# Optimization experiments

Measured on AMD Instinct MI355X. Metric: run time of the kernel, lower is better.

The kernel has to match this reference:

```python
import jax, jax.numpy as jnp
import numpy as np

B, S, H = 4, 2048, 1024
HEADS = 16
DFF = 4 * H
EPS = 1e-12


def _layer_norm(x, w, b):
    mu = jnp.mean(x, axis=-1, keepdims=True)
    var = jnp.mean(jnp.square(x - mu), axis=-1, keepdims=True)
    return (x - mu) * jax.lax.rsqrt(var + EPS) * w + b


def setup_inputs() -> dict:
    key = jax.random.key(0)
    ks = jax.random.split(key, 12)
    sc = 0.02
    return {
        "input": jax.random.normal(ks[0], (B, S, H), dtype=jnp.float32),
        "input_mask": jnp.zeros((B, 1, 1, S), dtype=jnp.float32),
        "norm_w": jnp.ones((H,), jnp.float32),
        "norm_b": jnp.zeros((H,), jnp.float32),
        "qkv_w": sc * jax.random.normal(ks[1], (H, 3 * H), jnp.float32),
        "qkv_b": jnp.zeros((3 * H,), jnp.float32),
        "attn_ow": sc * jax.random.normal(ks[2], (H, H), jnp.float32),
        "attn_ob": jnp.zeros((H,), jnp.float32),
        "attn_nw": jnp.ones((H,), jnp.float32),
        "attn_nb": jnp.zeros((H,), jnp.float32),
        "inter_w": sc * jax.random.normal(ks[3], (H, DFF), jnp.float32),
        "inter_b": jnp.zeros((DFF,), jnp.float32),
        "output_w": sc * jax.random.normal(ks[4], (DFF, H), jnp.float32),
        "output_b": jnp.zeros((H,), jnp.float32),
    }


def reference(input, input_mask, norm_w, norm_b, qkv_w, qkv_b, attn_ow, attn_ob,
              attn_nw, attn_nb, inter_w, inter_b, output_w, output_b):
    b, s, h = input.shape
    hd = h // HEADS
    # pre-LN + fused QKV projection (qkv_func)
    x_ln = _layer_norm(input, norm_w, norm_b)
    qkv = x_ln @ qkv_w + qkv_b                      # [b, s, 3h]
    qkv = qkv.reshape(b, s, 3, HEADS, hd)
    q, k, v = qkv[:, :, 0], qkv[:, :, 1], qkv[:, :, 2]   # [b, s, heads, hd]
    # scaled dot-product attention (flash_attn equivalent, non-causal)
    scale = 1.0 / jnp.sqrt(jnp.float32(hd))
    scores = jnp.einsum('bqnd,bknd->bnqk', q, k) * scale  # [b, heads, s, s]
    scores = scores + input_mask                           # additive mask
    probs = jax.nn.softmax(scores, axis=-1)
    ctx = jnp.einsum('bnqk,bknd->bqnd', probs, v).reshape(b, s, h)
    # attention output projection + residual (mlp_func first half)
    attn_out = ctx @ attn_ow + attn_ob + input
    # post-attention LN + FFN (GELU) + residual
    y = _layer_norm(attn_out, attn_nw, attn_nb)
    y = jax.nn.gelu(y @ inter_w + inter_b, approximate=False)
    return y @ output_w + output_b + attn_out
```

## Files before the change

kernel.cpp:

```cpp
#include <hip/hip_runtime.h>
#include <math.h>

typedef __bf16 bf16_t;
typedef bf16_t bf16x8 __attribute__((ext_vector_type(8)));
typedef bf16_t bf16x4 __attribute__((ext_vector_type(4)));
typedef float f32x4 __attribute__((ext_vector_type(4)));
typedef float f32x16 __attribute__((ext_vector_type(16)));

#define BB 4
#define SS 2048
#define HD1 1024
#define NH 16
#define DFF_ 4096

__device__ __forceinline__ void gload_lds16(const bf16_t* g, bf16_t* l) {
  __builtin_amdgcn_global_load_lds(
      (const __attribute__((address_space(1))) void*)g,
      (__attribute__((address_space(3))) void*)l, 16, 0, 0);
}

__device__ __forceinline__ unsigned pack2_bf16(float a, float b) {
  union { bf16_t h[2]; unsigned u; } cv;
  cv.h[0] = (bf16_t)a;
  cv.h[1] = (bf16_t)b;
  return cv.u;
}

__device__ __forceinline__ float block_reduce_sum(float v, float* red) {
  const int lane = threadIdx.x & 63;
  const int wid = threadIdx.x >> 6;
#pragma unroll
  for (int off = 32; off > 0; off >>= 1) v += __shfl_down(v, off, 64);
  if (lane == 0) red[wid] = v;
  __syncthreads();
  float s = red[0] + red[1] + red[2] + red[3];
  __syncthreads();
  return s;
}

__global__ __launch_bounds__(256) void ln_kernel(const float* __restrict__ x,
                                                 const float* __restrict__ w,
                                                 const float* __restrict__ bv,
                                                 bf16_t* __restrict__ out) {
  __shared__ float red[4];
  const size_t row = blockIdx.x;
  const float4 xv = *(const float4*)(x + row * HD1 + threadIdx.x * 4);
  float s = xv.x + xv.y + xv.z + xv.w;
  s = block_reduce_sum(s, red);
  const float mu = s * (1.0f / HD1);
  float4 d;
  d.x = xv.x - mu; d.y = xv.y - mu; d.z = xv.z - mu; d.w = xv.w - mu;
  float sq = d.x * d.x + d.y * d.y + d.z * d.z + d.w * d.w;
  sq = block_reduce_sum(sq, red);
  const float rs = rsqrtf(sq * (1.0f / HD1) + 1e-12f);
  const float4 wv = *(const float4*)(w + threadIdx.x * 4);
  const float4 bb = *(const float4*)(bv + threadIdx.x * 4);
  bf16x4 o;
  o[0] = (bf16_t)(d.x * rs * wv.x + bb.x);
  o[1] = (bf16_t)(d.y * rs * wv.y + bb.y);
  o[2] = (bf16_t)(d.z * rs * wv.z + bb.z);
  o[3] = (bf16_t)(d.w * rs * wv.w + bb.w);
  *(bf16x4*)(out + row * HD1 + threadIdx.x * 4) = o;
}

__global__ __launch_bounds__(256) void wt_kernel(const float* __restrict__ W,
                                                 bf16_t* __restrict__ Wt,
                                                 int K, int N) {
  __shared__ bf16_t T[32][33];
  const int t = threadIdx.x;
  const int n0 = blockIdx.x * 32, k0 = blockIdx.y * 32;
  const int a = t >> 5, c = t & 31;
#pragma unroll
  for (int i = 0; i < 4; ++i) {
    const int kl = a + i * 8;
    T[kl][c] = (bf16_t)W[(size_t)(k0 + kl) * N + n0 + c];
  }
  __syncthreads();
#pragma unroll
  for (int i = 0; i < 4; ++i) {
    const int nl = a + i * 8;
    Wt[(size_t)(n0 + nl) * K + k0 + c] = T[c][nl];
  }
}

__global__ __launch_bounds__(256) void vtrans_kernel(const bf16_t* __restrict__ qkv,
                                                     bf16_t* __restrict__ Vt) {
  const int t = threadIdx.x;
  const int s = blockIdx.x * 256 + t;
  const int head = blockIdx.y, b = blockIdx.z;
  const bf16_t* src = qkv + (size_t)(b * SS + s) * 3072 + 2048 + head * 64;
  bf16_t* dst = Vt + ((size_t)(b * NH + head) * 64) * SS + s;
#pragma unroll
  for (int j = 0; j < 8; ++j) {
    bf16x8 v = *(const bf16x8*)(src + j * 8);
#pragma unroll
    for (int e = 0; e < 8; ++e) dst[(size_t)(j * 8 + e) * SS] = v[e];
  }
}

template <int EPI, bool OBF>
__global__ __launch_bounds__(256) void gemm_bf16(
    const bf16_t* __restrict__ A, const bf16_t* __restrict__ Wt,
    const float* __restrict__ bias, const float* __restrict__ R,
    void* __restrict__ Cout, int M, int N, int K) {
  __shared__ __align__(16) char smem[65536];
  bf16_t* As = (bf16_t*)smem;
  bf16_t* Bs = (bf16_t*)(smem + 32768);
  const int tid = threadIdx.x;
  const int lane = tid & 63;
  const int w = tid >> 6;
  const int wm = (w >> 1) * 64, wn = (w & 1) * 64;
  const int l15 = lane & 15, l4 = lane >> 4;

  const int gx = gridDim.x;
  int id = blockIdx.x + gx * blockIdx.y;
  const int cpx = (gx * gridDim.y) >> 3;
  id = (id & 7) * cpx + (id >> 3);
  const int m0 = (id / gx) * 128;
  const int n0 = (id % gx) * 128;

  const int lrow = tid >> 3;
  const int lcol = (((tid & 7) ^ ((tid >> 3) & 7)) * 8);
  const bf16_t* Ag = A + (size_t)(m0 + lrow) * K + lcol;
  const bf16_t* Bg = Wt + (size_t)(n0 + lrow) * K + lcol;
  const size_t rstride = (size_t)32 * K;

#pragma unroll
  for (int c = 0; c < 4; ++c) {
    gload_lds16(Ag + c * rstride, As + c * 2048 + w * 512);
    gload_lds16(Bg + c * rstride, Bs + c * 2048 + w * 512);
  }

  const int NT = K >> 6;
  f32x4 acc[4][4] = {};

  const int ch0 = (((0 * 4 + l4) ^ (l15 & 7)) * 8);
  const int ch1 = (((1 * 4 + l4) ^ (l15 & 7)) * 8);

  for (int t = 0; t < NT; ++t) {
    const int cur = t & 1;
    __syncthreads();
    if (t + 1 < NT) {
      const bf16_t* Agn = Ag + (size_t)(t + 1) * 64;
      const bf16_t* Bgn = Bg + (size_t)(t + 1) * 64;
      bf16_t* Ad = As + (cur ^ 1) * 8192;
      bf16_t* Bd = Bs + (cur ^ 1) * 8192;
#pragma unroll
      for (int c = 0; c < 4; ++c) {
        gload_lds16(Agn + c * rstride, Ad + c * 2048 + w * 512);
        gload_lds16(Bgn + c * rstride, Bd + c * 2048 + w * 512);
      }
    }
    const bf16_t* Ab = As + cur * 8192;
    const bf16_t* Bb = Bs + cur * 8192;
    bf16x8 af[2][4], bfr[2][4];
#pragma unroll
    for (int i = 0; i < 4; ++i) {
      af[0][i] = *(const bf16x8*)(Ab + (wm + i * 16 + l15) * 64 + ch0);
      af[1][i] = *(const bf16x8*)(Ab + (wm + i * 16 + l15) * 64 + ch1);
    }
#pragma unroll
    for (int j = 0; j < 4; ++j) {
      bfr[0][j] = *(const bf16x8*)(Bb + (wn + j * 16 + l15) * 64 + ch0);
      bfr[1][j] = *(const bf16x8*)(Bb + (wn + j * 16 + l15) * 64 + ch1);
    }
#pragma unroll
    for (int ks = 0; ks < 2; ++ks)
#pragma unroll
      for (int i = 0; i < 4; ++i)
#pragma unroll
        for (int j = 0; j < 4; ++j)
          acc[i][j] = __builtin_amdgcn_mfma_f32_16x16x32_bf16(
              af[ks][i], bfr[ks][j], acc[i][j], 0, 0, 0);
  }

  if (OBF) {
    __syncthreads();
    float* Cs = (float*)smem;
#pragma unroll
    for (int j = 0; j < 4; ++j) {
      const float bj = bias[n0 + wn + j * 16 + l15];
#pragma unroll
      for (int i = 0; i < 4; ++i)
#pragma unroll
        for (int r = 0; r < 4; ++r) {
          float v = acc[i][j][r] + bj;
          if (EPI == 1)
            v = 0.5f * v * (1.0f + erff(v * 0.70710678118654752440f));
          Cs[(wm + i * 16 + l4 * 4 + r) * 128 + wn + j * 16 + l15] = v;
        }
    }
    __syncthreads();
    bf16_t* Cb = (bf16_t*)Cout;
#pragma unroll
    for (int p = 0; p < 16; ++p) {
      const int idx = p * 256 + tid;
      const int row = idx >> 5, c4 = idx & 31;
      const f32x4 v = *(const f32x4*)(Cs + row * 128 + c4 * 4);
      bf16x4 o;
      o[0] = (bf16_t)v[0]; o[1] = (bf16_t)v[1];
      o[2] = (bf16_t)v[2]; o[3] = (bf16_t)v[3];
      *(bf16x4*)(Cb + (size_t)(m0 + row) * N + n0 + c4 * 4) = o;
    }
  } else {
    float* Cf = (float*)Cout;
#pragma unroll
    for (int j = 0; j < 4; ++j) {
      const int gn = n0 + wn + j * 16 + l15;
      const float bj = bias[gn];
#pragma unroll
      for (int i = 0; i < 4; ++i) {
        const int gm = m0 + wm + i * 16 + l4 * 4;
#pragma unroll
        for (int r = 0; r < 4; ++r) {
          float v = acc[i][j][r] + bj;
          if (EPI == 2) v += R[(size_t)(gm + r) * N + gn];
          Cf[(size_t)(gm + r) * N + gn] = v;
        }
      }
    }
  }
}

__global__ __launch_bounds__(256, 3) void attn_kernel(
    const bf16_t* __restrict__ qkv, const bf16_t* __restrict__ Vt,
    const float* __restrict__ mask, bf16_t* __restrict__ ctx) {
  __shared__ __align__(16) bf16_t K_lds[64 * 72];
  __shared__ __align__(16) bf16_t Vt_lds[64 * 72];
  const int tid = threadIdx.x;
  const int lane = tid & 63;
  const int w = tid >> 6;
  const int l31 = lane & 31;
  const int h = lane >> 5;
  const int q0 = blockIdx.x * 128;
  const int head = blockIdx.y;
  const int b = blockIdx.z;
  const int qrow = q0 + w * 32 + l31;

  bf16x8 qf[4];
  {
    const bf16_t* qp = qkv + (size_t)(b * SS + qrow) * 3072 + head * 64 + 8 * h;
#pragma unroll
    for (int ks = 0; ks < 4; ++ks) qf[ks] = *(const bf16x8*)(qp + 16 * ks);
  }

  const int srow = tid >> 2;
  const int scol = (tid & 3) * 16;
  const float* mbase = mask + (size_t)b * SS;

  float m = -3.0e38f, l = 0.0f;
  f32x16 cacc0 = {};
  f32x16 cacc1 = {};

  for (int kv0 = 0; kv0 < SS; kv0 += 64) {
    const bf16_t* kp =
        qkv + (size_t)(b * SS + kv0 + srow) * 3072 + 1024 + head * 64 + scol;
    const bf16_t* vp =
        Vt + ((size_t)(b * NH + head) * 64 + srow) * SS + kv0 + scol;
    const bf16x8 k0 = *(const bf16x8*)kp;
    const bf16x8 k1 = *(const bf16x8*)(kp + 8);
    const bf16x8 v0 = *(const bf16x8*)vp;
    const bf16x8 v1 = *(const bf16x8*)(vp + 8);
    __syncthreads();
    *(bf16x8*)(K_lds + srow * 72 + scol) = k0;
    *(bf16x8*)(K_lds + srow * 72 + scol + 8) = k1;
    *(bf16x8*)(Vt_lds + srow * 72 + scol) = v0;
    *(bf16x8*)(Vt_lds + srow * 72 + scol + 8) = v1;
    __syncthreads();

    f32x16 sacc0 = {};
    f32x16 sacc1 = {};
#pragma unroll
    for (int ks = 0; ks < 4; ++ks) {
      const bf16x8 kf0 = *(const bf16x8*)(K_lds + l31 * 72 + 16 * ks + 8 * h);
      const bf16x8 kf1 =
          *(const bf16x8*)(K_lds + (l31 + 32) * 72 + 16 * ks + 8 * h);
      sacc0 = __builtin_amdgcn_mfma_f32_32x32x16_bf16(kf0, qf[ks], sacc0, 0, 0, 0);
      sacc1 = __builtin_amdgcn_mfma_f32_32x32x16_bf16(kf1, qf[ks], sacc1, 0, 0, 0);
    }

    float ps[32];
    float tmax = -3.0e38f;
#pragma unroll
    for (int r = 0; r < 16; ++r) {
      const int krow = (r & 3) + 8 * (r >> 2) + 4 * h;
      const float s0 = sacc0[r] * 0.125f + mbase[kv0 + krow];
      const float s1 = sacc1[r] * 0.125f + mbase[kv0 + 32 + krow];
      ps[r] = s0;
      ps[16 + r] = s1;
      tmax = fmaxf(tmax, fmaxf(s0, s1));
    }
    tmax = fmaxf(tmax, __shfl_xor(tmax, 32, 64));
    if (__any(tmax > m + 8.0f)) {
      const float mnew = fmaxf(m, tmax);
      const float sc = __expf(m - mnew);
      m = mnew;
      l *= sc;
#pragma unroll
      for (int r = 0; r < 16; ++r) {
        const float scr = __shfl(sc, (r & 3) + 8 * (r >> 2) + 4 * h, 64);
        cacc0[r] *= scr;
        cacc1[r] *= scr;
      }
    }
    float ls = 0.0f;
#pragma unroll
    for (int i = 0; i < 32; ++i) {
      ps[i] = __expf(ps[i] - m);
      ls += ps[i];
    }
    l += ls + __shfl_xor(ls, 32, 64);

    unsigned pw0[8], pw1[8];
#pragma unroll
    for (int k = 0; k < 8; ++k) {
      const int base = (k >> 2) * 16 + (k & 3) * 4;
      pw0[k] = pack2_bf16(ps[base + 0], ps[base + 1]);
      pw1[k] = pack2_bf16(ps[base + 2], ps[base + 3]);
    }
#pragma unroll
    for (int t = 0; t < 4; ++t) {
      const unsigned e0 = h ? pw0[2 * t] : pw0[2 * t + 1];
      const unsigned e1 = h ? pw1[2 * t] : pw1[2 * t + 1];
      const unsigned o0 = (unsigned)__shfl_xor((int)e0, 32, 64);
      const unsigned o1 = (unsigned)__shfl_xor((int)e1, 32, 64);
      const unsigned a0 = h ? pw0[2 * t + 1] : pw0[2 * t];
      const unsigned a1 = h ? pw1[2 * t + 1] : pw1[2 * t];
      union { unsigned u[4]; bf16x8 v; } pu;
      pu.u[0] = h ? o0 : a0;
      pu.u[1] = h ? o1 : a1;
      pu.u[2] = h ? a0 : o0;
      pu.u[3] = h ? a1 : o1;
      const bf16x8 vf0 = *(const bf16x8*)(Vt_lds + l31 * 72 + 16 * t + 8 * h);
      const bf16x8 vf1 =
          *(const bf16x8*)(Vt_lds + (l31 + 32) * 72 + 16 * t + 8 * h);
      cacc0 = __builtin_amdgcn_mfma_f32_32x32x16_bf16(pu.v, vf0, cacc0, 0, 0, 0);
      cacc1 = __builtin_amdgcn_mfma_f32_32x32x16_bf16(pu.v, vf1, cacc1, 0, 0, 0);
    }
  }

  const float linv = 1.0f / l;
#pragma unroll
  for (int r = 0; r < 16; ++r) {
    const int rq = (r & 3) + 8 * (r >> 2) + 4 * h;
    const float li = __shfl(linv, rq, 64);
    const int grow = q0 + w * 32 + rq;
    bf16_t* op = ctx + (size_t)(b * SS + grow) * 1024 + head * 64 + l31;
    op[0] = (bf16_t)(cacc0[r] * li);
    op[32] = (bf16_t)(cacc1[r] * li);
  }
}

extern "C" void kernel_launch(void* const* d_in, const int* in_sizes, int n_in,
                              void* d_out, int out_size, void* d_ws, size_t ws_size,
                              hipStream_t stream) {
  const float* input    = (const float*)d_in[0];
  const float* mask     = (const float*)d_in[1];
  const float* norm_w   = (const float*)d_in[2];
  const float* norm_b   = (const float*)d_in[3];
  const float* qkv_w    = (const float*)d_in[4];
  const float* qkv_b    = (const float*)d_in[5];
  const float* attn_ow  = (const float*)d_in[6];
  const float* attn_ob  = (const float*)d_in[7];
  const float* attn_nw  = (const float*)d_in[8];
  const float* attn_nb  = (const float*)d_in[9];
  const float* inter_w  = (const float*)d_in[10];
  const float* inter_b  = (const float*)d_in[11];
  const float* output_w = (const float*)d_in[12];
  const float* output_b = (const float*)d_in[13];

  char* ws = (char*)d_ws;
  const size_t off_xln = 0;
  const size_t off_qkv = 16777216;
  const size_t off_vt  = 67108864;
  const size_t off_ctx = 83886080;
  const size_t off_ao  = 100663296;
  const size_t off_wq  = 134217728;
  const size_t off_wo  = 140509184;
  const size_t off_wi  = 142606336;
  const size_t off_w2  = 150994944;
  const size_t NEED    = 159383552;
  if (ws_size < NEED) return;

  bf16_t* x_ln  = (bf16_t*)(ws + off_xln);
  bf16_t* qkvb  = (bf16_t*)(ws + off_qkv);
  bf16_t* VtB   = (bf16_t*)(ws + off_vt);
  bf16_t* ctxb  = (bf16_t*)(ws + off_ctx);
  bf16_t* y_ln  = (bf16_t*)(ws + off_ctx);
  float*  a_out = (float*)(ws + off_ao);
  bf16_t* wq_t  = (bf16_t*)(ws + off_wq);
  bf16_t* wo_t  = (bf16_t*)(ws + off_wo);
  bf16_t* wi_t  = (bf16_t*)(ws + off_wi);
  bf16_t* w2_t  = (bf16_t*)(ws + off_w2);
  bf16_t* act   = (bf16_t*)(ws + off_xln);

  const int M = BB * SS;

  wt_kernel<<<dim3(3072 / 32, 1024 / 32), 256, 0, stream>>>(qkv_w, wq_t, 1024, 3072);
  wt_kernel<<<dim3(1024 / 32, 1024 / 32), 256, 0, stream>>>(attn_ow, wo_t, 1024, 1024);
  wt_kernel<<<dim3(4096 / 32, 1024 / 32), 256, 0, stream>>>(inter_w, wi_t, 1024, 4096);
  wt_kernel<<<dim3(1024 / 32, 4096 / 32), 256, 0, stream>>>(output_w, w2_t, 4096, 1024);

  ln_kernel<<<M, 256, 0, stream>>>(input, norm_w, norm_b, x_ln);
  gemm_bf16<0, true><<<dim3(3072 / 128, M / 128), 256, 0, stream>>>(
      x_ln, wq_t, qkv_b, nullptr, qkvb, M, 3072, 1024);
  vtrans_kernel<<<dim3(SS / 256, NH, BB), 256, 0, stream>>>(qkvb, VtB);
  attn_kernel<<<dim3(SS / 128, NH, BB), 256, 0, stream>>>(qkvb, VtB, mask, ctxb);
  gemm_bf16<2, false><<<dim3(1024 / 128, M / 128), 256, 0, stream>>>(
      ctxb, wo_t, attn_ob, input, a_out, M, 1024, 1024);
  ln_kernel<<<M, 256, 0, stream>>>(a_out, attn_nw, attn_nb, y_ln);
  gemm_bf16<1, true><<<dim3(4096 / 128, M / 128), 256, 0, stream>>>(
      y_ln, wi_t, inter_b, nullptr, act, M, 4096, 1024);
  gemm_bf16<2, false><<<dim3(1024 / 128, M / 128), 256, 0, stream>>>(
      act, w2_t, output_b, a_out, (float*)d_out, M, 1024, 4096);
}
```

Baseline: 490.2 us.

## Prefetch K/V tiles into registers, vectorize mask loads, and tile V transpose through LDS

```diff
diff --git a/kernel.cpp b/kernel.cpp
--- a/kernel.cpp
+++ b/kernel.cpp
@@ -20,10 +20,9 @@
 }
 
 __device__ __forceinline__ unsigned pack2_bf16(float a, float b) {
-  union { bf16_t h[2]; unsigned u; } cv;
-  cv.h[0] = (bf16_t)a;
-  cv.h[1] = (bf16_t)b;
-  return cv.u;
+  unsigned r;
+  asm("v_cvt_pk_bf16_f32 %0, %1, %2" : "=v"(r) : "v"(a), "v"(b));
+  return r;
 }
 
 __device__ __forceinline__ float block_reduce_sum(float v, float* red) {
@@ -85,16 +84,32 @@
 
 __global__ __launch_bounds__(256) void vtrans_kernel(const bf16_t* __restrict__ qkv,
                                                      bf16_t* __restrict__ Vt) {
+  __shared__ bf16_t T[256 * 66];
   const int t = threadIdx.x;
-  const int s = blockIdx.x * 256 + t;
+  const int s0 = blockIdx.x * 256;
   const int head = blockIdx.y, b = blockIdx.z;
-  const bf16_t* src = qkv + (size_t)(b * SS + s) * 3072 + 2048 + head * 64;
-  bf16_t* dst = Vt + ((size_t)(b * NH + head) * 64) * SS + s;
-#pragma unroll
-  for (int j = 0; j < 8; ++j) {
-    bf16x8 v = *(const bf16x8*)(src + j * 8);
-#pragma unroll
-    for (int e = 0; e < 8; ++e) dst[(size_t)(j * 8 + e) * SS] = v[e];
+  const int rr = t >> 3, dc = (t & 7) * 8;
+#pragma unroll
+  for (int p = 0; p < 8; ++p) {
+    const int s = rr + p * 32;
+    const bf16x8 v = *(const bf16x8*)(
+        qkv + (size_t)(b * SS + s0 + s) * 3072 + 2048 + head * 64 + dc);
+    *(bf16x8*)&T[s * 66 + dc] = v;
+  }
+  __syncthreads();
+  const int dd = t >> 3;
+  const int sw = (t & 7) * 8;
+#pragma unroll
+  for (int p = 0; p < 2; ++p) {
+    const int d = dd + p * 32;
+    bf16_t* dst = Vt + ((size_t)(b * NH + head) * 64 + d) * SS + s0;
+#pragma unroll
+    for (int j = 0; j < 4; ++j) {
+      bf16x8 o;
+#pragma unroll
+      for (int e = 0; e < 8; ++e) o[e] = T[(sw + j * 64 + e) * 66 + d];
+      *(bf16x8*)(dst + sw + j * 64) = o;
+    }
   }
 }
 
@@ -246,26 +261,37 @@
 
   const int srow = tid >> 2;
   const int scol = (tid & 3) * 16;
-  const float* mbase = mask + (size_t)b * SS;
+  const bf16_t* kp0 =
+      qkv + (size_t)(b * SS + srow) * 3072 + 1024 + head * 64 + scol;
+  const bf16_t* vp0 = Vt + ((size_t)(b * NH + head) * 64 + srow) * SS + scol;
+
+  bf16x8 kr0 = *(const bf16x8*)kp0;
+  bf16x8 kr1 = *(const bf16x8*)(kp0 + 8);
+  bf16x8 vr0 = *(const bf16x8*)vp0;
+  bf16x8 vr1 = *(const bf16x8*)(vp0 + 8);
 
   float m = -3.0e38f, l = 0.0f;
   f32x16 cacc0 = {};
   f32x16 cacc1 = {};
 
   for (int kv0 = 0; kv0 < SS; kv0 += 64) {
-    const bf16_t* kp =
-        qkv + (size_t)(b * SS + kv0 + srow) * 3072 + 1024 + head * 64 + scol;
-    const bf16_t* vp =
-        Vt + ((size_t)(b * NH + head) * 64 + srow) * SS + kv0 + scol;
-    const bf16x8 k0 = *(const bf16x8*)kp;
-    const bf16x8 k1 = *(const bf16x8*)(kp + 8);
-    const bf16x8 v0 = *(const bf16x8*)vp;
-    const bf16x8 v1 = *(const bf16x8*)(vp + 8);
     __syncthreads();
-    *(bf16x8*)(K_lds + srow * 72 + scol) = k0;
-    *(bf16x8*)(K_lds + srow * 72 + scol + 8) = k1;
-    *(bf16x8*)(Vt_lds + srow * 72 + scol) = v0;
-    *(bf16x8*)(Vt_lds + srow * 72 + scol + 8) = v1;
+    *(bf16x8*)(K_lds + srow * 72 + scol) = kr0;
+    *(bf16x8*)(K_lds + srow * 72 + scol + 8) = kr1;
+    *(bf16x8*)(Vt_lds + srow * 72 + scol) = vr0;
+    *(bf16x8*)(Vt_lds + srow * 72 + scol + 8) = vr1;
+    if (kv0 + 64 < SS) {
+      const bf16_t* kp = kp0 + (size_t)(kv0 + 64) * 3072;
+      const bf16_t* vp = vp0 + (kv0 + 64);
+      kr0 = *(const bf16x8*)kp;
+      kr1 = *(const bf16x8*)(kp + 8);
+      vr0 = *(const bf16x8*)vp;
+      vr1 = *(const bf16x8*)(vp + 8);
+    }
+    float4 mv[8];
+#pragma unroll
+    for (int k2 = 0; k2 < 8; ++k2)
+      mv[k2] = *(const float4*)(mask + (size_t)b * SS + kv0 + 8 * k2 + 4 * h);
     __syncthreads();
 
     f32x16 sacc0 = {};
@@ -283,9 +309,8 @@
     float tmax = -3.0e38f;
 #pragma unroll
     for (int r = 0; r < 16; ++r) {
-      const int krow = (r & 3) + 8 * (r >> 2) + 4 * h;
-      const float s0 = sacc0[r] * 0.125f + mbase[kv0 + krow];
-      const float s1 = sacc1[r] * 0.125f + mbase[kv0 + 32 + krow];
+      const float s0 = sacc0[r] * 0.125f + mv[(r >> 2)][r & 3];
+      const float s1 = sacc1[r] * 0.125f + mv[(r >> 2) + 4][r & 3];
       ps[r] = s0;
       ps[16 + r] = s1;
       tmax = fmaxf(tmax, fmaxf(s0, s1));
```

New measurement: 459.8 us. 6.2% less time.
